# Optimization experiments

Hardware: AMD Instinct MI355X
Metric: run time of the kernel (lower is better)

## Reference

```python
import jax, jax.numpy as jnp
import numpy as np
from jax import lax

B = 64            # batch size
IMG = 128         # image H=W
C_IN = 3          # channels (also conv kernel size in original code)
Q_DIM = 11
A_DIM = 10
CONV = [24, 24, 24, 24]
KS = 3
EPS = 1e-5
G_IN = (CONV[-1] + 2) * 2 + Q_DIM  # 63


def _lin_init(key, fin, fout):
    kw, kb = jax.random.split(key)
    w = jax.random.normal(kw, (fin, fout), jnp.float32) / np.sqrt(fin).astype(np.float32)
    b = jax.random.normal(kb, (fout,), jnp.float32) * 0.01
    return w, b


def _conv_init(key, cin, cout):
    kw, kb = jax.random.split(key)
    w = jax.random.normal(kw, (cout, cin, KS, KS), jnp.float32) / np.sqrt(cin * KS * KS).astype(np.float32)
    b = jax.random.normal(kb, (cout,), jnp.float32) * 0.01
    return w, b


def setup_inputs() -> dict:
    key = jax.random.key(0)
    ks = jax.random.split(key, 16)
    inp = {
        'img': jax.random.normal(ks[0], (B, C_IN, IMG, IMG), jnp.float32),
        'q': jax.random.normal(ks[1], (B, Q_DIM), jnp.float32),
    }
    cins = [C_IN] + CONV[:-1]
    for li in range(4):
        w, b = _conv_init(ks[2 + li], cins[li], CONV[li])
        inp[f'cw{li+1}'], inp[f'cb{li+1}'] = w, b
        inp[f'bg{li+1}'] = jnp.ones((CONV[li],), jnp.float32)
        inp[f'bb{li+1}'] = jnp.zeros((CONV[li],), jnp.float32)
    gins = [G_IN, 256, 256, 256]
    for li in range(4):
        w, b = _lin_init(ks[6 + li], gins[li], 256)
        inp[f'gw{li+1}'], inp[f'gb{li+1}'] = w, b
    fins, fouts = [256, 256, 256], [256, 256, A_DIM]
    for li in range(3):
        w, b = _lin_init(ks[10 + li], fins[li], fouts[li])
        inp[f'fw{li+1}'], inp[f'fb{li+1}'] = w, b
    return inp


def _conv_block(x, w, b, g, bb):
    # conv(stride=2, pad=1) -> relu -> batchnorm (train-mode batch stats)
    x = lax.conv_general_dilated(x, w, (2, 2), [(1, 1), (1, 1)],
                                 dimension_numbers=('NCHW', 'OIHW', 'NCHW'))
    x = jax.nn.relu(x + b[None, :, None, None])
    m = jnp.mean(x, axis=(0, 2, 3), keepdims=True)
    v = jnp.var(x, axis=(0, 2, 3), keepdims=True)
    return g[None, :, None, None] * (x - m) * jax.lax.rsqrt(v + EPS) + bb[None, :, None, None]


def _forward(img, q,
             cw1, cb1, bg1, bb1, cw2, cb2, bg2, bb2,
             cw3, cb3, bg3, bb3, cw4, cb4, bg4, bb4,
             gw1, gb1, gw2, gb2, gw3, gb3, gw4, gb4,
             fw1, fb1, fw2, fb2, fw3, fb3):
    x = _conv_block(img, cw1, cb1, bg1, bb1)
    x = _conv_block(x, cw2, cb2, bg2, bb2)
    x = _conv_block(x, cw3, cb3, bg3, bb3)
    x = _conv_block(x, cw4, cb4, bg4, bb4)        # [B, K, d, d]
    d = x.shape[2]
    N = d * d
    Kc = x.shape[1]
    # objects: o at flat index i corresponds to pixel (i//d, i%d) -> row-major reshape
    objs = x.reshape(B, Kc, N).transpose(0, 2, 1)           # [B, N, K]
    idx = jnp.arange(N)
    coords = jnp.stack([(idx // d).astype(jnp.float32) / d,
                        (idx % d).astype(jnp.float32) / d], axis=1)  # [N, 2]
    o = jnp.concatenate([objs, jnp.broadcast_to(coords[None], (B, N, 2))], axis=-1)  # [B, N, K+2]
    F = Kc + 2
    oi = jnp.broadcast_to(o[:, :, None, :], (B, N, N, F))
    oj = jnp.broadcast_to(o[:, None, :, :], (B, N, N, F))
    qb = jnp.broadcast_to(q[:, None, None, :], (B, N, N, Q_DIM))
    pair = jnp.concatenate([oi, oj, qb], axis=-1)           # [B, N, N, 2F+Q]
    h = jax.nn.relu(jnp.einsum('bijf,fh->bijh', pair, gw1) + gb1)
    h = jax.nn.relu(h @ gw2 + gb2)
    h = jax.nn.relu(h @ gw3 + gb3)
    h = jax.nn.relu(h @ gw4 + gb4)
    g = jnp.mean(h, axis=(1, 2))                            # mean over all N*N pairs -> [B, 256]
    # f_phi (dropout as identity / eval mode)
    g = jax.nn.relu(g @ fw1 + fb1)
    g = jax.nn.relu(g @ fw2 + fb2)
    logits = g @ fw3 + fb3
    return logits


def reference(img, q,
              cw1, cb1, bg1, bb1, cw2, cb2, bg2, bb2,
              cw3, cb3, bg3, bb3, cw4, cb4, bg4, bb4,
              gw1, gb1, gw2, gb2, gw3, gb3, gw4, gb4,
              fw1, fb1, fw2, fb2, fw3, fb3):
    return _forward(img, q,
                    cw1, cb1, bg1, bb1, cw2, cb2, bg2, bb2,
                    cw3, cb3, bg3, bb3, cw4, cb4, bg4, bb4,
                    gw1, gb1, gw2, gb2, gw3, gb3, gw4, gb4,
                    fw1, fb1, fw2, fb2, fw3, fb3)
```

## Files before the change

kernel.cpp:

```cpp
#include <hip/hip_runtime.h>
#include <hip/hip_bf16.h>

#define EPS_BN 1e-5f

typedef __bf16 bf16_t;
typedef __bf16 bf16x8 __attribute__((ext_vector_type(8)));
typedef float floatx16 __attribute__((ext_vector_type(16)));

__global__ __launch_bounds__(256) void prep_kernel(
    const float* __restrict__ q, const float* __restrict__ gw1,
    const float* __restrict__ gb1, const float* __restrict__ g2,
    const float* __restrict__ g3, const float* __restrict__ g4,
    float* __restrict__ wq, bf16_t* __restrict__ wpack)
{
    int blk = blockIdx.x, t = threadIdx.x;
    {
        float acc = gb1[t];
        #pragma unroll
        for (int d = 0; d < 11; d++)
            acc = fmaf(q[blk * 11 + d], gw1[(52 + d) * 256 + t], acc);
        wq[blk * 256 + t] = acc;
    }
    for (int idx = blk * 3072 + t; idx < blk * 3072 + 3072; idx += 256) {
        int layer = idx >> 16;
        int rem = idx & 65535;
        int col = rem & 255;
        int k = rem >> 8;
        const float* gw = (layer == 0) ? g2 : ((layer == 1) ? g3 : g4);
        float v = gw[k * 256 + col];
        int cg = col >> 5, l31 = col & 31;
        int kt = k >> 4, l2 = (k >> 3) & 1, e = k & 7;
        int lane = l2 * 32 + l31;
        wpack[(((layer * 8 + cg) * 16 + kt) * 64 + lane) * 8 + e] = (bf16_t)v;
    }
}

__global__ __launch_bounds__(256) void fin_kernel(
    const float* __restrict__ part, int P, float inv_n,
    const float* __restrict__ gamma, const float* __restrict__ beta,
    float* __restrict__ scsh)
{
    int c = blockIdx.x;
    int t = threadIdx.x;
    float s1 = 0.f, s2 = 0.f;
    for (int p = t; p < P; p += 256) {
        s1 += part[p * 48 + 2 * c];
        s2 += part[p * 48 + 2 * c + 1];
    }
    #pragma unroll
    for (int off = 32; off > 0; off >>= 1) {
        s1 += __shfl_xor(s1, off);
        s2 += __shfl_xor(s2, off);
    }
    __shared__ float r1[4], r2[4];
    int lane = t & 63, w = t >> 6;
    if (lane == 0) { r1[w] = s1; r2[w] = s2; }
    __syncthreads();
    if (t == 0) {
        float a1 = r1[0] + r1[1] + r1[2] + r1[3];
        float a2 = r2[0] + r2[1] + r2[2] + r2[3];
        float m = a1 * inv_n;
        float var = a2 * inv_n - m * m;
        float sc = gamma[c] * rsqrtf(var + EPS_BN);
        scsh[c] = sc;
        scsh[24 + c] = fmaf(-m, sc, beta[c]);
    }
}

template<int CIN, int HOUT, int OY_PER, int CO_PER, bool FOLD>
__global__ __launch_bounds__(256) void conv_kernel(
    const float* __restrict__ in, const float* __restrict__ scsh_in,
    const float* __restrict__ w, const float* __restrict__ bias,
    float* __restrict__ out, float* __restrict__ part_out)
{
    const int HIN = 2 * HOUT, ROWS = 2 * OY_PER + 3, RW = 2 * HOUT + 2;
    const int TILES = HOUT / OY_PER;
    const int WPC = (HOUT * OY_PER) / 64;
    int b = blockIdx.x / TILES, tile = blockIdx.x % TILES;
    int oy0 = tile * OY_PER;
    __shared__ float tin[CIN][ROWS][RW];
    __shared__ float scf[24], shf[24];
    __shared__ float red[4][CO_PER * 2];
    int t = threadIdx.x;
    if (FOLD) {
        if (t < 24) { scf[t] = scsh_in[t]; shf[t] = scsh_in[24 + t]; }
        __syncthreads();
    }
    const int total = CIN * ROWS * RW;
    int iyb = 2 * oy0 - 1;
    #pragma unroll 2
    for (int idx = t; idx < total; idx += 256) {
        int rx = idx % RW;
        int rem = idx / RW;
        int ry = rem % ROWS;
        int ci = rem / ROWS;
        int iy = iyb + ry, ix = rx - 1;
        float v = 0.f;
        if ((unsigned)iy < (unsigned)HIN && (unsigned)ix < (unsigned)HIN) {
            float raw = in[(b * CIN + ci) * HIN * HIN + iy * HIN + ix];
            v = FOLD ? fmaf(raw, scf[ci], shf[ci]) : raw;
        }
        tin[ci][ry][rx] = v;
    }
    __syncthreads();
    int ox = t % HOUT;
    int oyl = (t / HOUT) % OY_PER;
    int cog = t / (HOUT * OY_PER);
    const float* wp = w + cog * CO_PER * CIN * 9;
    float acc[CO_PER];
    #pragma unroll
    for (int r = 0; r < CO_PER; r++) acc[r] = bias[cog * CO_PER + r];
    for (int ci = 0; ci < CIN; ci++)
        #pragma unroll
        for (int ky = 0; ky < 3; ky++)
            #pragma unroll
            for (int kx = 0; kx < 3; kx++) {
                float v = tin[ci][2 * oyl + ky][2 * ox + kx];
                #pragma unroll
                for (int r = 0; r < CO_PER; r++)
                    acc[r] = fmaf(v, wp[(r * CIN + ci) * 9 + ky * 3 + kx], acc[r]);
            }
    int oy = oy0 + oyl;
    float s1[CO_PER], s2[CO_PER];
    #pragma unroll
    for (int r = 0; r < CO_PER; r++) {
        float v = fmaxf(acc[r], 0.f);
        out[((b * 24 + cog * CO_PER + r) * HOUT + oy) * HOUT + ox] = v;
        s1[r] = v;
        s2[r] = v * v;
    }
    int lane = t & 63, w_id = t >> 6;
    #pragma unroll
    for (int r = 0; r < CO_PER; r++) {
        float a = s1[r], c2 = s2[r];
        #pragma unroll
        for (int off = 32; off > 0; off >>= 1) {
            a += __shfl_xor(a, off);
            c2 += __shfl_xor(c2, off);
        }
        if (lane == 0) { red[w_id][r * 2] = a; red[w_id][r * 2 + 1] = c2; }
    }
    __syncthreads();
    if (t < 48) {
        int ch = t >> 1, st = t & 1;
        int cg = ch / CO_PER, r = ch % CO_PER;
        float v = 0.f;
        #pragma unroll
        for (int k = 0; k < WPC; k++) v += red[cg * WPC + k][r * 2 + st];
        part_out[blockIdx.x * 48 + t] = v;
    }
}

__global__ __launch_bounds__(256) void uv_kernel(
    const float* __restrict__ x4, const float* __restrict__ scsh4,
    const float* __restrict__ gw1, float* __restrict__ U, float* __restrict__ V)
{
    int b = blockIdx.x >> 2, n0 = (blockIdx.x & 3) * 16;
    __shared__ float o[16][26];
    int t = threadIdx.x;
    for (int idx = t; idx < 16 * 26; idx += 256) {
        int n = idx / 26, f = idx % 26;
        int ng = n0 + n;
        float val;
        if (f < 24)
            val = fmaf(x4[(b * 24 + f) * 64 + ng], scsh4[f], scsh4[24 + f]);
        else if (f == 24) val = (float)(ng >> 3) * 0.125f;
        else              val = (float)(ng & 7) * 0.125f;
        o[n][f] = val;
    }
    __syncthreads();
    float g1u[26], g1v[26];
    #pragma unroll
    for (int f = 0; f < 26; f++) {
        g1u[f] = gw1[f * 256 + t];
        g1v[f] = gw1[(26 + f) * 256 + t];
    }
    for (int n = 0; n < 16; n++) {
        float u = 0.f, v = 0.f;
        #pragma unroll
        for (int f = 0; f < 26; f++) {
            float of = o[n][f];
            u = fmaf(of, g1u[f], u);
            v = fmaf(of, g1v[f], v);
        }
        int ng = n0 + n;
        U[(b * 64 + ng) * 256 + t] = u;
        V[(b * 64 + ng) * 256 + t] = v;
    }
}

__global__ __launch_bounds__(512, 4) void pair_kernel(
    const float* __restrict__ U, const float* __restrict__ V,
    const float* __restrict__ wq, const bf16_t* __restrict__ wpack,
    const float* __restrict__ gb2, const float* __restrict__ gb3,
    const float* __restrict__ gb4, float* __restrict__ partial)
{
    __shared__ __align__(16) bf16_t hA[128][264];
    __shared__ float csum[2][256];
    int blk = blockIdx.x;
    int b = blk >> 5;
    int i0 = (blk & 31) * 2;
    int t = threadIdx.x;

    {
        int c = t & 255, jh = t >> 8;
        float wqc = wq[b * 256 + c];
        float uw0 = U[(b * 64 + i0) * 256 + c] + wqc;
        float uw1 = U[(b * 64 + i0 + 1) * 256 + c] + wqc;
        const float* Vb = V + (b * 64) * 256;
        for (int j = jh * 32; j < jh * 32 + 32; j++) {
            float v = Vb[j * 256 + c];
            hA[j][c]      = (bf16_t)fmaxf(uw0 + v, 0.0f);
            hA[64 + j][c] = (bf16_t)fmaxf(uw1 + v, 0.0f);
        }
    }
    __syncthreads();

    int lane = t & 63, wave = t >> 6;
    int wm = wave >> 2, wn = wave & 3;
    int l31 = lane & 31, l2 = lane >> 5;
    int r0 = wm * 64 + l31;
    const floatx16 zero16 = {0.f, 0.f, 0.f, 0.f, 0.f, 0.f, 0.f, 0.f,
                             0.f, 0.f, 0.f, 0.f, 0.f, 0.f, 0.f, 0.f};
    float colsum[2] = {0.f, 0.f};

    #pragma unroll 1
    for (int layer = 0; layer < 3; layer++) {
        const float* bias = (layer == 0) ? gb2 : ((layer == 1) ? gb3 : gb4);
        float bcol[2];
        #pragma unroll
        for (int nt = 0; nt < 2; nt++)
            bcol[nt] = bias[wn * 64 + nt * 32 + l31];

        floatx16 acc[2][2];
        #pragma unroll
        for (int mt = 0; mt < 2; mt++)
            #pragma unroll
            for (int nt = 0; nt < 2; nt++) acc[mt][nt] = zero16;

        const bf16_t* W0 = wpack + ((size_t)(layer * 8 + wn * 2) * 16 * 64 + lane) * 8;
        const bf16_t* W1 = W0 + (size_t)16 * 64 * 8;
        bf16x8 Bc[2];
        Bc[0] = *(const bf16x8*)W0;
        Bc[1] = *(const bf16x8*)W1;

        #pragma unroll
        for (int ks = 0; ks < 16; ks++) {
            bf16x8 Bn[2];
            if (ks < 15) {
                Bn[0] = *(const bf16x8*)(W0 + (ks + 1) * 64 * 8);
                Bn[1] = *(const bf16x8*)(W1 + (ks + 1) * 64 * 8);
            }
            bf16x8 a0 = *(const bf16x8*)&hA[r0][ks * 16 + l2 * 8];
            bf16x8 a1 = *(const bf16x8*)&hA[r0 + 32][ks * 16 + l2 * 8];
            #pragma unroll
            for (int nt = 0; nt < 2; nt++) {
                acc[0][nt] = __builtin_amdgcn_mfma_f32_32x32x16_bf16(a0, Bc[nt], acc[0][nt], 0, 0, 0);
                acc[1][nt] = __builtin_amdgcn_mfma_f32_32x32x16_bf16(a1, Bc[nt], acc[1][nt], 0, 0, 0);
            }
            if (ks < 15) { Bc[0] = Bn[0]; Bc[1] = Bn[1]; }
        }

        if (layer < 2) {
            __syncthreads();
            #pragma unroll
            for (int mt = 0; mt < 2; mt++)
                #pragma unroll
                for (int nt = 0; nt < 2; nt++) {
                    int col = wn * 64 + nt * 32 + l31;
                    #pragma unroll
                    for (int reg = 0; reg < 16; reg++) {
                        int row = wm * 64 + mt * 32 + (reg & 3) + 8 * (reg >> 2) + 4 * l2;
                        hA[row][col] = (bf16_t)fmaxf(acc[mt][nt][reg] + bcol[nt], 0.0f);
                    }
                }
            __syncthreads();
        } else {
            #pragma unroll
            for (int nt = 0; nt < 2; nt++) {
                float s = 0.f;
                #pragma unroll
                for (int mt = 0; mt < 2; mt++)
                    #pragma unroll
                    for (int reg = 0; reg < 16; reg++)
                        s += fmaxf(acc[mt][nt][reg] + bcol[nt], 0.0f);
                colsum[nt] += s;
            }
        }
    }

    #pragma unroll
    for (int nt = 0; nt < 2; nt++)
        colsum[nt] += __shfl_xor(colsum[nt], 32);
    if (l2 == 0) {
        #pragma unroll
        for (int nt = 0; nt < 2; nt++)
            csum[wm][wn * 64 + nt * 32 + l31] = colsum[nt];
    }
    __syncthreads();
    if (t < 256)
        partial[blk * 256 + t] = csum[0][t] + csum[1][t];
}

__global__ __launch_bounds__(256) void fphi_kernel(
    const float* __restrict__ partial,
    const float* __restrict__ fw1, const float* __restrict__ fb1,
    const float* __restrict__ fw2, const float* __restrict__ fb2,
    const float* __restrict__ fw3, const float* __restrict__ fb3,
    float* __restrict__ out)
{
    int b = blockIdx.x, t = threadIdx.x;
    __shared__ float g[256], h1[256], h2[256];
    float s = 0.f;
    for (int k = 0; k < 32; k++) s += partial[(b * 32 + k) * 256 + t];
    g[t] = s * (1.0f / 4096.0f);
    __syncthreads();
    float a1 = fb1[t];
    for (int k = 0; k < 256; k++) a1 = fmaf(g[k], fw1[k * 256 + t], a1);
    h1[t] = fmaxf(a1, 0.0f);
    __syncthreads();
    float a2 = fb2[t];
    for (int k = 0; k < 256; k++) a2 = fmaf(h1[k], fw2[k * 256 + t], a2);
    h2[t] = fmaxf(a2, 0.0f);
    __syncthreads();
    if (t < 10) {
        float a3 = fb3[t];
        for (int k = 0; k < 256; k++) a3 = fmaf(h2[k], fw3[k * 10 + t], a3);
        out[b * 10 + t] = a3;
    }
}

extern "C" void kernel_launch(void* const* d_in, const int* in_sizes, int n_in,
                              void* d_out, int out_size, void* d_ws, size_t ws_size,
                              hipStream_t stream)
{
    (void)in_sizes; (void)n_in; (void)out_size; (void)ws_size;
    const float* img = (const float*)d_in[0];
    const float* q   = (const float*)d_in[1];
    const float* cw[4] = {(const float*)d_in[2],  (const float*)d_in[6],
                          (const float*)d_in[10], (const float*)d_in[14]};
    const float* cb[4] = {(const float*)d_in[3],  (const float*)d_in[7],
                          (const float*)d_in[11], (const float*)d_in[15]};
    const float* bg[4] = {(const float*)d_in[4],  (const float*)d_in[8],
                          (const float*)d_in[12], (const float*)d_in[16]};
    const float* bbv[4] = {(const float*)d_in[5],  (const float*)d_in[9],
                           (const float*)d_in[13], (const float*)d_in[17]};
    const float* gw1 = (const float*)d_in[18]; const float* gb1 = (const float*)d_in[19];
    const float* gw2 = (const float*)d_in[20]; const float* gb2 = (const float*)d_in[21];
    const float* gw3 = (const float*)d_in[22]; const float* gb3 = (const float*)d_in[23];
    const float* gw4 = (const float*)d_in[24]; const float* gb4 = (const float*)d_in[25];
    const float* fw1 = (const float*)d_in[26]; const float* fb1 = (const float*)d_in[27];
    const float* fw2 = (const float*)d_in[28]; const float* fb2 = (const float*)d_in[29];
    const float* fw3 = (const float*)d_in[30]; const float* fb3 = (const float*)d_in[31];

    float* ws  = (float*)d_ws;
    float* x1  = ws;
    float* x2  = x1 + 6291456;
    float* x3  = x2 + 1572864;
    float* x4  = x3 + 393216;
    float* U   = x4 + 98304;
    float* V   = U + 1048576;
    float* wqv = V + 1048576;
    float* part = wqv + 16384;
    float* p1  = part + 524288;
    float* p2  = p1 + 98304;
    float* p3  = p2 + 49152;
    float* p4  = p3 + 12288;
    float* scsh1 = p4 + 3072;
    float* scsh2 = scsh1 + 48;
    float* scsh3 = scsh2 + 48;
    float* scsh4 = scsh3 + 48;
    bf16_t* wpack = (bf16_t*)(scsh4 + 48);

    prep_kernel<<<64, 256, 0, stream>>>(q, gw1, gb1, gw2, gw3, gw4, wqv, wpack);
    conv_kernel<3, 64, 2, 12, false><<<2048, 256, 0, stream>>>(
        img, nullptr, cw[0], cb[0], x1, p1);
    fin_kernel<<<24, 256, 0, stream>>>(p1, 2048, 1.f / 262144.f, bg[0], bbv[0], scsh1);
    conv_kernel<24, 32, 2, 6, true><<<1024, 256, 0, stream>>>(
        x1, scsh1, cw[1], cb[1], x2, p2);
    fin_kernel<<<24, 256, 0, stream>>>(p2, 1024, 1.f / 65536.f, bg[1], bbv[1], scsh2);
    conv_kernel<24, 16, 4, 6, true><<<256, 256, 0, stream>>>(
        x2, scsh2, cw[2], cb[2], x3, p3);
    fin_kernel<<<24, 256, 0, stream>>>(p3, 256, 1.f / 16384.f, bg[2], bbv[2], scsh3);
    conv_kernel<24, 8, 8, 6, true><<<64, 256, 0, stream>>>(
        x3, scsh3, cw[3], cb[3], x4, p4);
    fin_kernel<<<24, 256, 0, stream>>>(p4, 64, 1.f / 4096.f, bg[3], bbv[3], scsh4);
    uv_kernel<<<256, 256, 0, stream>>>(x4, scsh4, gw1, U, V);
    pair_kernel<<<2048, 512, 0, stream>>>(U, V, wqv, wpack, gb2, gb3, gb4, part);
    fphi_kernel<<<64, 256, 0, stream>>>(part, fw1, fb1, fw2, fb2, fw3, fb3,
                                        (float*)d_out);
}
```

Baseline: 421.3 us.

## Fuse BN stat finalize into consumers and vectorize pair kernel LDS traffic

```diff
diff --git a/kernel.cpp b/kernel.cpp
--- a/kernel.cpp
+++ b/kernel.cpp
@@ -5,13 +5,17 @@
 
 typedef __bf16 bf16_t;
 typedef __bf16 bf16x8 __attribute__((ext_vector_type(8)));
+typedef __bf16 bf16x4 __attribute__((ext_vector_type(4)));
+typedef float fx4 __attribute__((ext_vector_type(4)));
 typedef float floatx16 __attribute__((ext_vector_type(16)));
 
 __global__ __launch_bounds__(256) void prep_kernel(
     const float* __restrict__ q, const float* __restrict__ gw1,
     const float* __restrict__ gb1, const float* __restrict__ g2,
     const float* __restrict__ g3, const float* __restrict__ g4,
-    float* __restrict__ wq, bf16_t* __restrict__ wpack)
+    const float* __restrict__ gb2, const float* __restrict__ gb3,
+    float* __restrict__ wq, bf16_t* __restrict__ wpack,
+    float* __restrict__ biaspack)
 {
     int blk = blockIdx.x, t = threadIdx.x;
     {
@@ -20,6 +24,15 @@
         for (int d = 0; d < 11; d++)
             acc = fmaf(q[blk * 11 + d], gw1[(52 + d) * 256 + t], acc);
         wq[blk * 256 + t] = acc;
+    }
+    if (blk == 0) {
+        for (int idx = t; idx < 512; idx += 256) {
+            int layer = idx >> 8;
+            int rem = idx & 255;
+            int cg = rem >> 5, l2 = (rem >> 4) & 1, reg = rem & 15;
+            int c = cg * 32 + (reg & 3) + 8 * (reg >> 2) + 4 * l2;
+            biaspack[idx] = (layer ? gb3 : gb2)[c];
+        }
     }
     for (int idx = blk * 3072 + t; idx < blk * 3072 + 3072; idx += 256) {
         int layer = idx >> 16;
@@ -35,43 +48,13 @@
     }
 }
 
-__global__ __launch_bounds__(256) void fin_kernel(
-    const float* __restrict__ part, int P, float inv_n,
-    const float* __restrict__ gamma, const float* __restrict__ beta,
-    float* __restrict__ scsh)
-{
-    int c = blockIdx.x;
-    int t = threadIdx.x;
-    float s1 = 0.f, s2 = 0.f;
-    for (int p = t; p < P; p += 256) {
-        s1 += part[p * 48 + 2 * c];
-        s2 += part[p * 48 + 2 * c + 1];
-    }
-    #pragma unroll
-    for (int off = 32; off > 0; off >>= 1) {
-        s1 += __shfl_xor(s1, off);
-        s2 += __shfl_xor(s2, off);
-    }
-    __shared__ float r1[4], r2[4];
-    int lane = t & 63, w = t >> 6;
-    if (lane == 0) { r1[w] = s1; r2[w] = s2; }
-    __syncthreads();
-    if (t == 0) {
-        float a1 = r1[0] + r1[1] + r1[2] + r1[3];
-        float a2 = r2[0] + r2[1] + r2[2] + r2[3];
-        float m = a1 * inv_n;
-        float var = a2 * inv_n - m * m;
-        float sc = gamma[c] * rsqrtf(var + EPS_BN);
-        scsh[c] = sc;
-        scsh[24 + c] = fmaf(-m, sc, beta[c]);
-    }
-}
-
-template<int CIN, int HOUT, int OY_PER, int CO_PER, bool FOLD>
+template<int CIN, int HOUT, int OY_PER, int CO_PER, int PSTAT>
 __global__ __launch_bounds__(256) void conv_kernel(
-    const float* __restrict__ in, const float* __restrict__ scsh_in,
-    const float* __restrict__ w, const float* __restrict__ bias,
-    float* __restrict__ out, float* __restrict__ part_out)
+    const float* __restrict__ in, const float* __restrict__ part_in,
+    float inv_n, const float* __restrict__ gamma,
+    const float* __restrict__ beta, const float* __restrict__ w,
+    const float* __restrict__ bias, float* __restrict__ out,
+    float* __restrict__ part_out)
 {
     const int HIN = 2 * HOUT, ROWS = 2 * OY_PER + 3, RW = 2 * HOUT + 2;
     const int TILES = HOUT / OY_PER;
@@ -80,10 +63,27 @@
     int oy0 = tile * OY_PER;
     __shared__ float tin[CIN][ROWS][RW];
     __shared__ float scf[24], shf[24];
+    __shared__ float fred[5][48];
     __shared__ float red[4][CO_PER * 2];
     int t = threadIdx.x;
-    if (FOLD) {
-        if (t < 24) { scf[t] = scsh_in[t]; shf[t] = scsh_in[24 + t]; }
+    if (PSTAT > 0) {
+        if (t < 240) {
+            int comp = t % 48, sl = t / 48;
+            float a = 0.f;
+            for (int p = sl; p < PSTAT; p += 5) a += part_in[p * 48 + comp];
+            fred[sl][comp] = a;
+        }
+        __syncthreads();
+        if (t < 24) {
+            float s1 = 0.f, s2 = 0.f;
+            #pragma unroll
+            for (int s = 0; s < 5; s++) { s1 += fred[s][2 * t]; s2 += fred[s][2 * t + 1]; }
+            float m = s1 * inv_n;
+            float var = s2 * inv_n - m * m;
+            float sc = gamma[t] * rsqrtf(var + EPS_BN);
+            scf[t] = sc;
+            shf[t] = fmaf(-m, sc, beta[t]);
+        }
         __syncthreads();
     }
     const int total = CIN * ROWS * RW;
@@ -98,7 +98,7 @@
         float v = 0.f;
         if ((unsigned)iy < (unsigned)HIN && (unsigned)ix < (unsigned)HIN) {
             float raw = in[(b * CIN + ci) * HIN * HIN + iy * HIN + ix];
-            v = FOLD ? fmaf(raw, scf[ci], shf[ci]) : raw;
+            v = (PSTAT > 0) ? fmaf(raw, scf[ci], shf[ci]) : raw;
         }
         tin[ci][ry][rx] = v;
     }
@@ -152,18 +152,39 @@
 }
 
 __global__ __launch_bounds__(256) void uv_kernel(
-    const float* __restrict__ x4, const float* __restrict__ scsh4,
+    const float* __restrict__ x4, const float* __restrict__ p4,
+    const float* __restrict__ g4, const float* __restrict__ b4,
     const float* __restrict__ gw1, float* __restrict__ U, float* __restrict__ V)
 {
     int b = blockIdx.x >> 2, n0 = (blockIdx.x & 3) * 16;
     __shared__ float o[16][26];
+    __shared__ float fred[5][48];
+    __shared__ float scf[24], shf[24];
     int t = threadIdx.x;
+    if (t < 240) {
+        int comp = t % 48, sl = t / 48;
+        float a = 0.f;
+        for (int p = sl; p < 64; p += 5) a += p4[p * 48 + comp];
+        fred[sl][comp] = a;
+    }
+    __syncthreads();
+    if (t < 24) {
+        float s1 = 0.f, s2 = 0.f;
+        #pragma unroll
+        for (int s = 0; s < 5; s++) { s1 += fred[s][2 * t]; s2 += fred[s][2 * t + 1]; }
+        float m = s1 * (1.f / 4096.f);
+        float var = s2 * (1.f / 4096.f) - m * m;
+        float sc = g4[t] * rsqrtf(var + EPS_BN);
+        scf[t] = sc;
+        shf[t] = fmaf(-m, sc, b4[t]);
+    }
+    __syncthreads();
     for (int idx = t; idx < 16 * 26; idx += 256) {
         int n = idx / 26, f = idx % 26;
         int ng = n0 + n;
         float val;
         if (f < 24)
-            val = fmaf(x4[(b * 24 + f) * 64 + ng], scsh4[f], scsh4[24 + f]);
+            val = fmaf(x4[(b * 24 + f) * 64 + ng], scf[f], shf[f]);
         else if (f == 24) val = (float)(ng >> 3) * 0.125f;
         else              val = (float)(ng & 7) * 0.125f;
         o[n][f] = val;
@@ -192,8 +213,8 @@
 __global__ __launch_bounds__(512, 4) void pair_kernel(
     const float* __restrict__ U, const float* __restrict__ V,
     const float* __restrict__ wq, const bf16_t* __restrict__ wpack,
-    const float* __restrict__ gb2, const float* __restrict__ gb3,
-    const float* __restrict__ gb4, float* __restrict__ partial)
+    const float* __restrict__ biaspack, const float* __restrict__ gb4,
+    float* __restrict__ partial)
 {
     __shared__ __align__(16) bf16_t hA[128][264];
     __shared__ float csum[2][256];
@@ -203,99 +224,138 @@
     int t = threadIdx.x;
 
     {
-        int c = t & 255, jh = t >> 8;
-        float wqc = wq[b * 256 + c];
-        float uw0 = U[(b * 64 + i0) * 256 + c] + wqc;
-        float uw1 = U[(b * 64 + i0 + 1) * 256 + c] + wqc;
-        const float* Vb = V + (b * 64) * 256;
-        for (int j = jh * 32; j < jh * 32 + 32; j++) {
-            float v = Vb[j * 256 + c];
-            hA[j][c]      = (bf16_t)fmaxf(uw0 + v, 0.0f);
-            hA[64 + j][c] = (bf16_t)fmaxf(uw1 + v, 0.0f);
+        int cc = t & 31, jg = t >> 5;
+        int c0 = cc * 8;
+        int ii = jg >> 3;
+        const float* Ub = U + (b * 64 + i0 + ii) * 256 + c0;
+        const float* Qb = wq + b * 256 + c0;
+        fx4 u0 = *(const fx4*)Ub + *(const fx4*)Qb;
+        fx4 u1 = *(const fx4*)(Ub + 4) + *(const fx4*)(Qb + 4);
+        const float* Vb = V + (b * 64) * 256 + c0;
+        int jbase = jg * 8;
+        #pragma unroll
+        for (int r = 0; r < 8; r++) {
+            int j = jbase + r;
+            const float* Vr = Vb + (j & 63) * 256;
+            fx4 v0 = *(const fx4*)Vr + u0;
+            fx4 v1 = *(const fx4*)(Vr + 4) + u1;
+            bf16x8 o;
+            #pragma unroll
+            for (int e = 0; e < 4; e++) {
+                o[e]     = (bf16_t)fmaxf(v0[e], 0.f);
+                o[e + 4] = (bf16_t)fmaxf(v1[e], 0.f);
+            }
+            *(bf16x8*)&hA[j][c0] = o;
         }
     }
     __syncthreads();
 
     int lane = t & 63, wave = t >> 6;
-    int wm = wave >> 2, wn = wave & 3;
     int l31 = lane & 31, l2 = lane >> 5;
-    int r0 = wm * 64 + l31;
     const floatx16 zero16 = {0.f, 0.f, 0.f, 0.f, 0.f, 0.f, 0.f, 0.f,
                              0.f, 0.f, 0.f, 0.f, 0.f, 0.f, 0.f, 0.f};
+
+    int cm = wave & 3, jn = wave >> 2;
+    #pragma unroll 1
+    for (int lay = 0; lay < 2; lay++) {
+        floatx16 acc[2][2];
+        #pragma unroll
+        for (int mt = 0; mt < 2; mt++)
+            #pragma unroll
+            for (int nt = 0; nt < 2; nt++) acc[mt][nt] = zero16;
+
+        const bf16_t* W0 = wpack + ((size_t)(lay * 8 + cm * 2) * 16 * 64 + lane) * 8;
+        const bf16_t* W1 = W0 + (size_t)16 * 64 * 8;
+        bf16x8 Ac[2];
+        Ac[0] = *(const bf16x8*)W0;
+        Ac[1] = *(const bf16x8*)W1;
+
+        #pragma unroll
+        for (int ks = 0; ks < 16; ks++) {
+            bf16x8 An[2];
+            if (ks < 15) {
+                An[0] = *(const bf16x8*)(W0 + (ks + 1) * 64 * 8);
+                An[1] = *(const bf16x8*)(W1 + (ks + 1) * 64 * 8);
+            }
+            bf16x8 b0 = *(const bf16x8*)&hA[jn * 64 + l31][ks * 16 + l2 * 8];
+            bf16x8 b1 = *(const bf16x8*)&hA[jn * 64 + 32 + l31][ks * 16 + l2 * 8];
+            acc[0][0] = __builtin_amdgcn_mfma_f32_32x32x16_bf16(Ac[0], b0, acc[0][0], 0, 0, 0);
+            acc[0][1] = __builtin_amdgcn_mfma_f32_32x32x16_bf16(Ac[0], b1, acc[0][1], 0, 0, 0);
+            acc[1][0] = __builtin_amdgcn_mfma_f32_32x32x16_bf16(Ac[1], b0, acc[1][0], 0, 0, 0);
+            acc[1][1] = __builtin_amdgcn_mfma_f32_32x32x16_bf16(Ac[1], b1, acc[1][1], 0, 0, 0);
+            if (ks < 15) { Ac[0] = An[0]; Ac[1] = An[1]; }
+        }
+        __syncthreads();
+        #pragma unroll
+        for (int mt = 0; mt < 2; mt++) {
+            const fx4* bp = (const fx4*)(biaspack + lay * 256 + (cm * 2 + mt) * 32 + l2 * 16);
+            fx4 bv[4];
+            #pragma unroll
+            for (int g = 0; g < 4; g++) bv[g] = bp[g];
+            int cb = cm * 64 + mt * 32 + 4 * l2;
+            #pragma unroll
+            for (int nt = 0; nt < 2; nt++) {
+                int j = jn * 64 + nt * 32 + l31;
+                #pragma unroll
+                for (int g = 0; g < 4; g++) {
+                    bf16x4 o;
+                    #pragma unroll
+                    for (int r = 0; r < 4; r++)
+                        o[r] = (bf16_t)fmaxf(acc[mt][nt][g * 4 + r] + bv[g][r], 0.f);
+                    *(bf16x4*)&hA[j][cb + 8 * g] = o;
+                }
+            }
+        }
+        __syncthreads();
+    }
+
+    int rm = wave >> 2, cn = wave & 3;
     float colsum[2] = {0.f, 0.f};
-
-    #pragma unroll 1
-    for (int layer = 0; layer < 3; layer++) {
-        const float* bias = (layer == 0) ? gb2 : ((layer == 1) ? gb3 : gb4);
-        float bcol[2];
-        #pragma unroll
-        for (int nt = 0; nt < 2; nt++)
-            bcol[nt] = bias[wn * 64 + nt * 32 + l31];
-
+    {
+        float bcol[2] = {gb4[cn * 64 + l31], gb4[cn * 64 + 32 + l31]};
         floatx16 acc[2][2];
         #pragma unroll
         for (int mt = 0; mt < 2; mt++)
             #pragma unroll
             for (int nt = 0; nt < 2; nt++) acc[mt][nt] = zero16;
-
-        const bf16_t* W0 = wpack + ((size_t)(layer * 8 + wn * 2) * 16 * 64 + lane) * 8;
-        const bf16_t* W1 = W0 + (size_t)16 * 64 * 8;
+        const bf16_t* B0 = wpack + ((size_t)(16 + cn * 2) * 16 * 64 + lane) * 8;
+        const bf16_t* B1 = B0 + (size_t)16 * 64 * 8;
         bf16x8 Bc[2];
-        Bc[0] = *(const bf16x8*)W0;
-        Bc[1] = *(const bf16x8*)W1;
-
+        Bc[0] = *(const bf16x8*)B0;
+        Bc[1] = *(const bf16x8*)B1;
         #pragma unroll
         for (int ks = 0; ks < 16; ks++) {
             bf16x8 Bn[2];
             if (ks < 15) {
-                Bn[0] = *(const bf16x8*)(W0 + (ks + 1) * 64 * 8);
-                Bn[1] = *(const bf16x8*)(W1 + (ks + 1) * 64 * 8);
+                Bn[0] = *(const bf16x8*)(B0 + (ks + 1) * 64 * 8);
+                Bn[1] = *(const bf16x8*)(B1 + (ks + 1) * 64 * 8);
             }
-            bf16x8 a0 = *(const bf16x8*)&hA[r0][ks * 16 + l2 * 8];
-            bf16x8 a1 = *(const bf16x8*)&hA[r0 + 32][ks * 16 + l2 * 8];
-            #pragma unroll
-            for (int nt = 0; nt < 2; nt++) {
-                acc[0][nt] = __builtin_amdgcn_mfma_f32_32x32x16_bf16(a0, Bc[nt], acc[0][nt], 0, 0, 0);
-                acc[1][nt] = __builtin_amdgcn_mfma_f32_32x32x16_bf16(a1, Bc[nt], acc[1][nt], 0, 0, 0);
-            }
+            bf16x8 a0 = *(const bf16x8*)&hA[rm * 64 + l31][ks * 16 + l2 * 8];
+            bf16x8 a1 = *(const bf16x8*)&hA[rm * 64 + 32 + l31][ks * 16 + l2 * 8];
+            acc[0][0] = __builtin_amdgcn_mfma_f32_32x32x16_bf16(a0, Bc[0], acc[0][0], 0, 0, 0);
+            acc[1][0] = __builtin_amdgcn_mfma_f32_32x32x16_bf16(a1, Bc[0], acc[1][0], 0, 0, 0);
+            acc[0][1] = __builtin_amdgcn_mfma_f32_32x32x16_bf16(a0, Bc[1], acc[0][1], 0, 0, 0);
+            acc[1][1] = __builtin_amdgcn_mfma_f32_32x32x16_bf16(a1, Bc[1], acc[1][1], 0, 0, 0);
             if (ks < 15) { Bc[0] = Bn[0]; Bc[1] = Bn[1]; }
         }
-
-        if (layer < 2) {
-            __syncthreads();
+        #pragma unroll
+        for (int nt = 0; nt < 2; nt++) {
+            float s = 0.f;
             #pragma unroll
             for (int mt = 0; mt < 2; mt++)
                 #pragma unroll
-                for (int nt = 0; nt < 2; nt++) {
-                    int col = wn * 64 + nt * 32 + l31;
-                    #pragma unroll
-                    for (int reg = 0; reg < 16; reg++) {
-                        int row = wm * 64 + mt * 32 + (reg & 3) + 8 * (reg >> 2) + 4 * l2;
-                        hA[row][col] = (bf16_t)fmaxf(acc[mt][nt][reg] + bcol[nt], 0.0f);
-                    }
-                }
-            __syncthreads();
-        } else {
-            #pragma unroll
-            for (int nt = 0; nt < 2; nt++) {
-                float s = 0.f;
-                #pragma unroll
-                for (int mt = 0; mt < 2; mt++)
-                    #pragma unroll
-                    for (int reg = 0; reg < 16; reg++)
-                        s += fmaxf(acc[mt][nt][reg] + bcol[nt], 0.0f);
-                colsum[nt] += s;
-            }
-        }
-    }
-
+                for (int reg = 0; reg < 16; reg++)
+                    s += fmaxf(acc[mt][nt][reg] + bcol[nt], 0.0f);
+            colsum[nt] += s;
+        }
+    }
     #pragma unroll
     for (int nt = 0; nt < 2; nt++)
         colsum[nt] += __shfl_xor(colsum[nt], 32);
     if (l2 == 0) {
         #pragma unroll
         for (int nt = 0; nt < 2; nt++)
-            csum[wm][wn * 64 + nt * 32 + l31] = colsum[nt];
+            csum[rm][cn * 64 + nt * 32 + l31] = colsum[nt];
     }
     __syncthreads();
     if (t < 256)
@@ -366,27 +426,21 @@
     float* p2  = p1 + 98304;
     float* p3  = p2 + 49152;
     float* p4  = p3 + 12288;
-    float* scsh1 = p4 + 3072;
-    float* scsh2 = scsh1 + 48;
-    float* scsh3 = scsh2 + 48;
-    float* scsh4 = scsh3 + 48;
-    bf16_t* wpack = (bf16_t*)(scsh4 + 48);
-
-    prep_kernel<<<64, 256, 0, stream>>>(q, gw1, gb1, gw2, gw3, gw4, wqv, wpack);
-    conv_kernel<3, 64, 2, 12, false><<<2048, 256, 0, stream>>>(
-        img, nullptr, cw[0], cb[0], x1, p1);
-    fin_kernel<<<24, 256, 0, stream>>>(p1, 2048, 1.f / 262144.f, bg[0], bbv[0], scsh1);
-    conv_kernel<24, 32, 2, 6, true><<<1024, 256, 0, stream>>>(
-        x1, scsh1, cw[1], cb[1], x2, p2);
-    fin_kernel<<<24, 256, 0, stream>>>(p2, 1024, 1.f / 65536.f, bg[1], bbv[1], scsh2);
-    conv_kernel<24, 16, 4, 6, true><<<256, 256, 0, stream>>>(
-        x2, scsh2, cw[2], cb[2], x3, p3);
-    fin_kernel<<<24, 256, 0, stream>>>(p3, 256, 1.f / 16384.f, bg[2], bbv[2], scsh3);
-    conv_kernel<24, 8, 8, 6, true><<<64, 256, 0, stream>>>(
-        x3, scsh3, cw[3], cb[3], x4, p4);
-    fin_kernel<<<24, 256, 0, stream>>>(p4, 64, 1.f / 4096.f, bg[3], bbv[3], scsh4);
-    uv_kernel<<<256, 256, 0, stream>>>(x4, scsh4, gw1, U, V);
-    pair_kernel<<<2048, 512, 0, stream>>>(U, V, wqv, wpack, gb2, gb3, gb4, part);
+    float* biaspack = p4 + 3072;
+    bf16_t* wpack = (bf16_t*)(biaspack + 512);
+
+    prep_kernel<<<64, 256, 0, stream>>>(q, gw1, gb1, gw2, gw3, gw4, gb2, gb3,
+                                        wqv, wpack, biaspack);
+    conv_kernel<3, 64, 2, 12, 0><<<2048, 256, 0, stream>>>(
+        img, nullptr, 0.f, nullptr, nullptr, cw[0], cb[0], x1, p1);
+    conv_kernel<24, 32, 2, 6, 2048><<<1024, 256, 0, stream>>>(
+        x1, p1, 1.f / 262144.f, bg[0], bbv[0], cw[1], cb[1], x2, p2);
+    conv_kernel<24, 16, 4, 6, 1024><<<256, 256, 0, stream>>>(
+        x2, p2, 1.f / 65536.f, bg[1], bbv[1], cw[2], cb[2], x3, p3);
+    conv_kernel<24, 8, 8, 6, 256><<<64, 256, 0, stream>>>(
+        x3, p3, 1.f / 16384.f, bg[2], bbv[2], cw[3], cb[3], x4, p4);
+    uv_kernel<<<256, 256, 0, stream>>>(x4, p4, bg[3], bbv[3], gw1, U, V);
+    pair_kernel<<<2048, 512, 0, stream>>>(U, V, wqv, wpack, biaspack, gb4, part);
     fphi_kernel<<<64, 256, 0, stream>>>(part, fw1, fb1, fw2, fb2, fw3, fb3,
                                         (float*)d_out);
 }
```

Result: slower. 614.3 us (+45.8%).
